# Optimization experiments

Measured on AMD Instinct MI355X. Metric: run time of the kernel, lower is better.

## Reference

```python
import jax, jax.numpy as jnp
import numpy as np

V_NUM = 4
NUM_HEADS = 8


def setup_inputs() -> dict:
    key = jax.random.key(0)
    k1, k2, k3 = jax.random.split(key, 3)
    B, C, H, W = 8, 512, 24, 24
    x = jax.random.normal(k1, (B, C, H, W), dtype=jnp.float32)
    # 1x1 conv weights stored as [out_ch, in_ch]
    w_qkv = jax.random.normal(k2, (3 * C, C), dtype=jnp.float32) * (C ** -0.5)
    w_proj = jax.random.normal(k3, (C, C), dtype=jnp.float32) * (C ** -0.5)
    b_proj = jnp.zeros((C,), dtype=jnp.float32)
    return {"x": x, "w_qkv": w_qkv, "w_proj": w_proj, "b_proj": b_proj}


def reference(x, w_qkv, w_proj, b_proj):
    B, C, H, W = x.shape
    hd = C // NUM_HEADS          # head dim
    scale = hd ** -0.5
    g = B // V_NUM               # batch groups
    N = V_NUM * H * W            # tokens per group

    # 1x1 conv qkv (no bias): [B, 3C, H, W]
    qkv = jnp.einsum('bchw,oc->bohw', x, w_qkv)
    # [g, v, 3C, H, W] -> [g, 3C, v, H, W] -> [g, heads, 3*hd, N]
    t = qkv.reshape(g, V_NUM, 3 * C, H, W).transpose(0, 2, 1, 3, 4)
    t = t.reshape(g, NUM_HEADS, 3 * hd, N)
    q, k, v = jnp.split(t, 3, axis=2)  # each [g, heads, hd, N]

    # attn = k^T @ q * scale : [g, heads, N, N]
    attn = jnp.einsum('ghdn,ghdm->ghnm', k, q) * scale
    attn = jax.nn.softmax(attn, axis=-2)  # softmax over the k axis (dim=-2)

    # out = v @ attn : [g, heads, hd, N]
    out = jnp.einsum('ghdn,ghnm->ghdm', v, attn)
    # [g, C, v, H, W] -> [g, v, C, H, W] -> [B, C, H, W]
    out = out.reshape(g, C, V_NUM, H, W).transpose(0, 2, 1, 3, 4).reshape(B, C, H, W)

    # 1x1 conv proj with bias
    out = jnp.einsum('bchw,oc->bohw', out, w_proj) + b_proj[None, :, None, None]
    return out
```

## Files before the change

### kernel.cpp

```cpp
#include <hip/hip_runtime.h>
#include <stdint.h>

typedef _Float16 f16;
typedef _Float16 half8 __attribute__((ext_vector_type(8)));
typedef _Float16 half4 __attribute__((ext_vector_type(4)));
typedef float floatx4 __attribute__((ext_vector_type(4)));

#define LOG2E 1.44269504088896340736f

__device__ __forceinline__ void async_cp16(const void* g, void* l) {
  __builtin_amdgcn_global_load_lds((const __attribute__((address_space(1))) void*)g,
                                   (__attribute__((address_space(3))) void*)l, 16, 0, 0);
}

__global__ __launch_bounds__(256) void k_prep(const float* __restrict__ x,
                                              f16* __restrict__ XT,
                                              const float* __restrict__ wqkv,
                                              const float* __restrict__ wproj,
                                              f16* __restrict__ WQ, f16* __restrict__ WP) {
  __shared__ f16 sT[64][72];
  const int bid = blockIdx.x;
  const int tid = threadIdx.x;
  if (bid < 576) {
    const int hw0 = (bid % 9) * 64, c0 = ((bid / 9) & 7) * 64, b = bid / 72;
    const int cc = tid >> 6, hwc = tid & 63;
    const float* xb = x + (size_t)b * 294912;
    for (int i = 0; i < 16; ++i) {
      int c = c0 + i * 4 + cc;
      sT[hwc][i * 4 + cc] = (f16)xb[c * 576 + hw0 + hwc];
    }
    __syncthreads();
    const int c_c = tid & 63, rr = tid >> 6;
    f16* xtb = XT + ((size_t)b * 576 + hw0) * 512 + c0;
    for (int j = 0; j < 16; ++j) {
      int r = j * 4 + rr;
      xtb[(size_t)r * 512 + c_c] = sT[r][c_c];
    }
  } else {
    const float SCALE_Q = 0.125f * LOG2E;
    const int total1 = 1536 * 512, total2 = 512 * 512;
    for (int idx = (bid - 576) * 256 + tid; idx < total1 + total2; idx += 128 * 256) {
      if (idx < total1) {
        int row = idx >> 9;
        float v = wqkv[idx];
        if ((row % 192) < 64) v *= SCALE_Q;
        WQ[idx] = (f16)v;
      } else {
        WP[idx - total1] = (f16)wproj[idx - total1];
      }
    }
  }
}

__global__ __launch_bounds__(256) void k_qkv_gemm(const f16* __restrict__ XT,
                                                  const f16* __restrict__ WQ,
                                                  f16* __restrict__ Qh, f16* __restrict__ Kh,
                                                  f16* __restrict__ Vh) {
  const int t0 = blockIdx.x * 128, n0 = blockIdx.y * 128;
  __shared__ alignas(16) f16 smem[2 * 128 * 64];
  f16* sA = smem;
  f16* sB = smem + 128 * 64;
  const int tid = threadIdx.x;
  const int wave = tid >> 6, lane = tid & 63, quad = lane >> 4, l16 = lane & 15;
  const int msub = (wave & 1) * 64, nsub = (wave >> 1) * 64;
  const floatx4 fzero = {0.f, 0.f, 0.f, 0.f};
  floatx4 acc[4][4];
  for (int i = 0; i < 4; ++i)
    for (int j = 0; j < 4; ++j) acc[i][j] = fzero;

  for (int k0 = 0; k0 < 512; k0 += 64) {
    __syncthreads();
    for (int p = 0; p < 4; ++p) {
      int e = p * 256 + tid;
      int row = e >> 3, colb = e & 7;
      async_cp16((const char*)XT + ((size_t)(t0 + row) * 512 + k0 + colb * 8) * 2,
                 (char*)sA + e * 16);
      async_cp16((const char*)WQ + ((size_t)(n0 + row) * 512 + k0 + colb * 8) * 2,
                 (char*)sB + e * 16);
    }
    __syncthreads();
    for (int f = 0; f < 2; ++f) {
      half8 a[4], bfr[4];
      for (int ms = 0; ms < 4; ++ms)
        a[ms] = *(const half8*)&sA[(msub + ms * 16 + l16) * 64 + f * 32 + quad * 8];
      for (int ns = 0; ns < 4; ++ns)
        bfr[ns] = *(const half8*)&sB[(nsub + ns * 16 + l16) * 64 + f * 32 + quad * 8];
      for (int ms = 0; ms < 4; ++ms)
        for (int ns = 0; ns < 4; ++ns)
          acc[ms][ns] =
              __builtin_amdgcn_mfma_f32_16x16x32_f16(a[ms], bfr[ns], acc[ms][ns], 0, 0, 0);
    }
  }
  for (int ms = 0; ms < 4; ++ms) {
    int tbase = t0 + msub + ms * 16 + quad * 4;
    for (int ns = 0; ns < 4; ++ns) {
      int row = n0 + nsub + ns * 16 + l16;
      int h = row / 192, rr2 = row % 192;
      int sel = rr2 >> 6, d = rr2 & 63;
      if (sel == 2) continue;
      for (int r = 0; r < 4; ++r) {
        int t = tbase + r;
        int b = t / 576, hw = t % 576;
        int g = b >> 2, v = b & 3;
        int n = v * 576 + hw;
        int gh = g * 8 + h;
        f16 hv = (f16)acc[ms][ns][r];
        size_t idx = ((size_t)gh * 2304 + n) * 64 + d;
        if (sel == 0)
          Qh[idx] = hv;
        else
          Kh[idx] = hv;
      }
    }
  }
  const int r0 = n0 % 192;
  if (r0 != 0) {
    const int vloc = (r0 == 128) ? 0 : 64;
    const int h = (n0 + vloc) / 192;
    f16* sVT = smem;
    __syncthreads();
    if ((wave >> 1) == (vloc >> 6)) {
      for (int ms = 0; ms < 4; ++ms) {
        int tok = msub + ms * 16 + quad * 4;
        for (int ns = 0; ns < 4; ++ns) {
          int d = ns * 16 + l16;
          half4 hv;
          for (int r = 0; r < 4; ++r) hv[r] = (f16)acc[ms][ns][r];
          *(half4*)&sVT[d * 136 + tok] = hv;
        }
      }
    }
    __syncthreads();
    for (int pss = 0; pss < 4; ++pss) {
      int d = pss * 16 + (tid >> 4), chunk = tid & 15;
      int t = t0 + chunk * 8;
      int b = t / 576, hw = t - b * 576;
      int gh = (b >> 2) * 8 + h, n = (b & 3) * 576 + hw;
      *(half8*)(Vh + (size_t)gh * 147456 + (size_t)d * 2304 + n) =
          *(const half8*)&sVT[d * 136 + chunk * 8];
    }
  }
}

__global__ __launch_bounds__(384) void k_attn(const f16* __restrict__ Qh,
                                              const f16* __restrict__ Kh,
                                              const f16* __restrict__ Vh,
                                              f16* __restrict__ AOT) {
  const int mt = blockIdx.x, gh = blockIdx.y;
  const int m0 = mt * 64;
  const int g = gh >> 3, h = gh & 7;
  const f16* Qg = Qh + (size_t)gh * 147456;
  const f16* Kg = Kh + (size_t)gh * 147456;
  const f16* Vg = Vh + (size_t)gh * 147456;
  __shared__ alignas(16) f16 smem[24576];
  f16* sK = smem;
  f16* sV = smem + 12288;
  const int tid = threadIdx.x;
  const int wave = tid >> 6, lane = tid & 63, quad = lane >> 4, l16 = lane & 15;
  const int wq = wave & 1, str = wave >> 1;
  const floatx4 fzero = {0.f, 0.f, 0.f, 0.f};
  const int sw = l16 & 7;
  const int vsw = (l16 >> 1) & 3;

  auto stage_kv = [&](int ktile, int buf) {
#pragma unroll
    for (int p = 0; p < 4; ++p) {
      int idx = p * 384 + tid;
      int isV = idx >= 768;
      int rem = isV ? idx - 768 : idx;
      int qt = rem >> 8, unit = rem & 255;
      if (!isV) {
        int row = unit >> 3, cb = unit & 7;
        async_cp16(Kg + (size_t)(qt * 768 + ktile * 32 + row) * 64 + ((cb ^ (row & 7)) << 3),
                   (char*)(sK + (qt * 2 + buf) * 2048) + unit * 16);
      } else {
        int row = unit >> 2, cb = unit & 3;
        async_cp16(
            Vg + (size_t)row * 2304 + qt * 768 + ktile * 32 + ((cb ^ ((row >> 1) & 3)) << 3),
            (char*)(sV + (qt * 2 + buf) * 2048) + unit * 16);
      }
    }
  };

  half8 qa[2][2];
#pragma unroll
  for (int s = 0; s < 2; ++s) {
    int qrow = m0 + wq * 32 + s * 16 + l16;
    qa[s][0] = *(const half8*)(Qg + (size_t)qrow * 64 + quad * 8);
    qa[s][1] = *(const half8*)(Qg + (size_t)qrow * 64 + 32 + quad * 8);
  }

  stage_kv(0, 0);
  __syncthreads();
  stage_kv(1, 1);

  float l_lane[2] = {0.f, 0.f};
  floatx4 o[2][4];
  for (int s = 0; s < 2; ++s)
    for (int dt = 0; dt < 4; ++dt) o[s][dt] = fzero;

  for (int kt = 0; kt < 24; ++kt) {
    const f16* bK = sK + (str * 2 + (kt & 1)) * 2048;
    const f16* bV = sV + (str * 2 + (kt & 1)) * 2048;

    half4 pf[2][2];
#pragma unroll
    for (int nt = 0; nt < 2; ++nt) {
      int krow = nt * 16 + l16;
      half8 kb0 = *(const half8*)&bK[krow * 64 + ((quad ^ sw) << 3)];
      half8 kb1 = *(const half8*)&bK[krow * 64 + (((4 + quad) ^ sw) << 3)];
#pragma unroll
      for (int s = 0; s < 2; ++s) {
        floatx4 t = __builtin_amdgcn_mfma_f32_16x16x32_f16(kb0, qa[s][0], fzero, 0, 0, 0);
        t = __builtin_amdgcn_mfma_f32_16x16x32_f16(kb1, qa[s][1], t, 0, 0, 0);
#pragma unroll
        for (int r = 0; r < 4; ++r) {
          float e = __builtin_amdgcn_exp2f(t[r]);
          l_lane[s] += e;
          pf[s][nt][r] = (f16)e;
        }
      }
    }
#pragma unroll
    for (int dt = 0; dt < 4; ++dt) {
      int vrow = dt * 16 + l16;
#pragma unroll
      for (int nt = 0; nt < 2; ++nt) {
        int chunk = nt * 2 + (quad >> 1);
        half4 vb = *(const half4*)&bV[vrow * 32 + ((chunk ^ vsw) << 3) + (quad & 1) * 4];
#pragma unroll
        for (int s = 0; s < 2; ++s)
          o[s][dt] = __builtin_amdgcn_mfma_f32_16x16x16f16(pf[s][nt], vb, o[s][dt], 0, 0, 0);
      }
    }

    if (kt < 23) {
      __syncthreads();
      if (kt + 2 < 24) stage_kv(kt + 2, kt & 1);
    }
  }

  __syncthreads();
  float* cO = (float*)smem;
  float* cL = (float*)(smem + 16384);
  if (str != 0) {
    int base = (str - 1) * 2 + wq;
#pragma unroll
    for (int s = 0; s < 2; ++s) {
      cL[(base * 2 + s) * 64 + lane] = l_lane[s];
      for (int dt = 0; dt < 4; ++dt)
        *(floatx4*)&cO[(((base * 2 + s) * 4 + dt) * 64 + lane) * 4] = o[s][dt];
    }
  }
  __syncthreads();
  if (str == 0) {
#pragma unroll
    for (int q2 = 0; q2 < 2; ++q2) {
      int base = q2 * 2 + wq;
      for (int s = 0; s < 2; ++s) {
        l_lane[s] += cL[(base * 2 + s) * 64 + lane];
        for (int dt = 0; dt < 4; ++dt)
          o[s][dt] += *(const floatx4*)&cO[(((base * 2 + s) * 4 + dt) * 64 + lane) * 4];
      }
    }
    for (int s = 0; s < 2; ++s) {
      l_lane[s] += __shfl_xor(l_lane[s], 16, 64);
      l_lane[s] += __shfl_xor(l_lane[s], 32, 64);
      float inv[4];
      for (int r = 0; r < 4; ++r) {
        float lr = __shfl(l_lane[s], quad * 4 + r, 64);
        inv[r] = 1.f / lr;
      }
      for (int dt = 0; dt < 4; ++dt)
        for (int r = 0; r < 4; ++r) {
          int n_tok = m0 + wq * 32 + s * 16 + quad * 4 + r;
          int v = n_tok / 576, hw = n_tok % 576;
          int bb = g * 4 + v;
          int c = h * 64 + dt * 16 + l16;
          AOT[((size_t)bb * 576 + hw) * 512 + c] = (f16)(o[s][dt][r] * inv[r]);
        }
    }
  }
}

__global__ __launch_bounds__(256) void k_proj_gemm(const f16* __restrict__ AOT,
                                                   const f16* __restrict__ WP,
                                                   const float* __restrict__ bias,
                                                   float* __restrict__ out) {
  const int o0 = blockIdx.x * 64, t0 = blockIdx.y * 128;
  __shared__ alignas(16) f16 sA[64 * 64];
  __shared__ alignas(16) f16 sB[128 * 64];
  const int tid = threadIdx.x;
  const int wave = tid >> 6, lane = tid & 63, quad = lane >> 4, l16 = lane & 15;
  const int msub = (wave & 1) * 32, nsub = (wave >> 1) * 64;
  const floatx4 fzero = {0.f, 0.f, 0.f, 0.f};
  floatx4 acc[2][4];
  for (int i = 0; i < 2; ++i)
    for (int j = 0; j < 4; ++j) acc[i][j] = fzero;

  for (int k0 = 0; k0 < 512; k0 += 64) {
    __syncthreads();
    for (int p = 0; p < 2; ++p) {
      int e = p * 256 + tid;
      int row = e >> 3, colb = e & 7;
      async_cp16((const char*)WP + ((size_t)(o0 + row) * 512 + k0 + colb * 8) * 2,
                 (char*)sA + e * 16);
    }
    for (int p = 0; p < 4; ++p) {
      int e = p * 256 + tid;
      int row = e >> 3, colb = e & 7;
      async_cp16((const char*)AOT + ((size_t)(t0 + row) * 512 + k0 + colb * 8) * 2,
                 (char*)sB + e * 16);
    }
    __syncthreads();
    for (int f = 0; f < 2; ++f) {
      half8 a[2], bfr[4];
      for (int ms = 0; ms < 2; ++ms)
        a[ms] = *(const half8*)&sA[(msub + ms * 16 + l16) * 64 + f * 32 + quad * 8];
      for (int ns = 0; ns < 4; ++ns)
        bfr[ns] = *(const half8*)&sB[(nsub + ns * 16 + l16) * 64 + f * 32 + quad * 8];
      for (int ms = 0; ms < 2; ++ms)
        for (int ns = 0; ns < 4; ++ns)
          acc[ms][ns] =
              __builtin_amdgcn_mfma_f32_16x16x32_f16(a[ms], bfr[ns], acc[ms][ns], 0, 0, 0);
    }
  }
  for (int ms = 0; ms < 2; ++ms) {
    int o_row = o0 + msub + ms * 16 + quad * 4;
    for (int ns = 0; ns < 4; ++ns) {
      int t = t0 + nsub + ns * 16 + l16;
      int b = t / 576, hw = t % 576;
      for (int r = 0; r < 4; ++r) {
        int orow = o_row + r;
        out[(size_t)b * 294912 + (size_t)orow * 576 + hw] = acc[ms][ns][r] + bias[orow];
      }
    }
  }
}

extern "C" void kernel_launch(void* const* d_in, const int* in_sizes, int n_in,
                              void* d_out, int out_size, void* d_ws, size_t ws_size,
                              hipStream_t stream) {
  const float* x = (const float*)d_in[0];
  const float* wqkv = (const float*)d_in[1];
  const float* wproj = (const float*)d_in[2];
  const float* bias = (const float*)d_in[3];
  float* out = (float*)d_out;
  char* ws = (char*)d_ws;
  f16* XT = (f16*)(ws + 0);
  f16* WQ = (f16*)(ws + 4718592);
  f16* WP = (f16*)(ws + 6291456);
  f16* Qh = (f16*)(ws + 6815744);
  f16* Kh = (f16*)(ws + 11534336);
  f16* Vh = (f16*)(ws + 16252928);
  f16* AOT = (f16*)(ws + 20971520);

  k_prep<<<dim3(704), dim3(256), 0, stream>>>(x, XT, wqkv, wproj, WQ, WP);
  k_qkv_gemm<<<dim3(36, 12), dim3(256), 0, stream>>>(XT, WQ, Qh, Kh, Vh);
  k_attn<<<dim3(36, 16), dim3(384), 0, stream>>>(Qh, Kh, Vh, AOT);
  k_proj_gemm<<<dim3(8, 36), dim3(256), 0, stream>>>(AOT, WP, bias, out);
}
```

Measured before the change: 156.7 us.

## Repartition attention block into 48-query tiles with two-way key split

Each attention block now handles 48 query rows split across three wave groups of 16 rows, with the key sequence split two ways instead of three, giving 768 blocks instead of 576. The goal is better CU occupancy and load balance on the device, plus a smaller LDS footprint per block. In exchange, each K/V tile loaded into LDS is reused by fewer query rows, so redundant K/V traffic rises. The longer serial loop over key tiles per wave also adds latency.

```diff
diff --git a/kernel.cpp b/kernel.cpp
--- a/kernel.cpp
+++ b/kernel.cpp
@@ -147,78 +147,76 @@
                                               const f16* __restrict__ Vh,
                                               f16* __restrict__ AOT) {
   const int mt = blockIdx.x, gh = blockIdx.y;
-  const int m0 = mt * 64;
+  const int m0 = mt * 48;
   const int g = gh >> 3, h = gh & 7;
   const f16* Qg = Qh + (size_t)gh * 147456;
   const f16* Kg = Kh + (size_t)gh * 147456;
   const f16* Vg = Vh + (size_t)gh * 147456;
-  __shared__ alignas(16) f16 smem[24576];
+  __shared__ alignas(16) f16 smem[16384];
   f16* sK = smem;
-  f16* sV = smem + 12288;
+  f16* sV = smem + 8192;
   const int tid = threadIdx.x;
   const int wave = tid >> 6, lane = tid & 63, quad = lane >> 4, l16 = lane & 15;
-  const int wq = wave & 1, str = wave >> 1;
+  const int str = wave & 1, qgrp = wave >> 1;
   const floatx4 fzero = {0.f, 0.f, 0.f, 0.f};
   const int sw = l16 & 7;
   const int vsw = (l16 >> 1) & 3;
 
   auto stage_kv = [&](int ktile, int buf) {
 #pragma unroll
-    for (int p = 0; p < 4; ++p) {
+    for (int p = 0; p < 3; ++p) {
       int idx = p * 384 + tid;
-      int isV = idx >= 768;
-      int rem = isV ? idx - 768 : idx;
-      int qt = rem >> 8, unit = rem & 255;
-      if (!isV) {
-        int row = unit >> 3, cb = unit & 7;
-        async_cp16(Kg + (size_t)(qt * 768 + ktile * 32 + row) * 64 + ((cb ^ (row & 7)) << 3),
-                   (char*)(sK + (qt * 2 + buf) * 2048) + unit * 16);
-      } else {
-        int row = unit >> 2, cb = unit & 3;
-        async_cp16(
-            Vg + (size_t)row * 2304 + qt * 768 + ktile * 32 + ((cb ^ ((row >> 1) & 3)) << 3),
-            (char*)(sV + (qt * 2 + buf) * 2048) + unit * 16);
+      if (idx < 1024) {
+        int isV = idx >= 512;
+        int rem = idx & 511;
+        int st = rem >> 8, unit = rem & 255;
+        if (!isV) {
+          int row = unit >> 3, cb = unit & 7;
+          async_cp16(
+              Kg + (size_t)(st * 1152 + ktile * 32 + row) * 64 + ((cb ^ (row & 7)) << 3),
+              (char*)(sK + (st * 2 + buf) * 2048) + unit * 16);
+        } else {
+          int row = unit >> 2, cb = unit & 3;
+          async_cp16(Vg + (size_t)row * 2304 + st * 1152 + ktile * 32 +
+                         ((cb ^ ((row >> 1) & 3)) << 3),
+                     (char*)(sV + (st * 2 + buf) * 2048) + unit * 16);
+        }
       }
     }
   };
 
-  half8 qa[2][2];
-#pragma unroll
-  for (int s = 0; s < 2; ++s) {
-    int qrow = m0 + wq * 32 + s * 16 + l16;
-    qa[s][0] = *(const half8*)(Qg + (size_t)qrow * 64 + quad * 8);
-    qa[s][1] = *(const half8*)(Qg + (size_t)qrow * 64 + 32 + quad * 8);
+  half8 qa[2];
+  {
+    int qrow = m0 + qgrp * 16 + l16;
+    qa[0] = *(const half8*)(Qg + (size_t)qrow * 64 + quad * 8);
+    qa[1] = *(const half8*)(Qg + (size_t)qrow * 64 + 32 + quad * 8);
   }
 
   stage_kv(0, 0);
   __syncthreads();
   stage_kv(1, 1);
 
-  float l_lane[2] = {0.f, 0.f};
-  floatx4 o[2][4];
-  for (int s = 0; s < 2; ++s)
-    for (int dt = 0; dt < 4; ++dt) o[s][dt] = fzero;
-
-  for (int kt = 0; kt < 24; ++kt) {
+  float l_lane = 0.f;
+  floatx4 o[4];
+  for (int dt = 0; dt < 4; ++dt) o[dt] = fzero;
+
+  for (int kt = 0; kt < 36; ++kt) {
     const f16* bK = sK + (str * 2 + (kt & 1)) * 2048;
     const f16* bV = sV + (str * 2 + (kt & 1)) * 2048;
 
-    half4 pf[2][2];
+    half4 pf[2];
 #pragma unroll
     for (int nt = 0; nt < 2; ++nt) {
       int krow = nt * 16 + l16;
       half8 kb0 = *(const half8*)&bK[krow * 64 + ((quad ^ sw) << 3)];
       half8 kb1 = *(const half8*)&bK[krow * 64 + (((4 + quad) ^ sw) << 3)];
-#pragma unroll
-      for (int s = 0; s < 2; ++s) {
-        floatx4 t = __builtin_amdgcn_mfma_f32_16x16x32_f16(kb0, qa[s][0], fzero, 0, 0, 0);
-        t = __builtin_amdgcn_mfma_f32_16x16x32_f16(kb1, qa[s][1], t, 0, 0, 0);
-#pragma unroll
-        for (int r = 0; r < 4; ++r) {
-          float e = __builtin_amdgcn_exp2f(t[r]);
-          l_lane[s] += e;
-          pf[s][nt][r] = (f16)e;
-        }
+      floatx4 t = __builtin_amdgcn_mfma_f32_16x16x32_f16(kb0, qa[0], fzero, 0, 0, 0);
+      t = __builtin_amdgcn_mfma_f32_16x16x32_f16(kb1, qa[1], t, 0, 0, 0);
+#pragma unroll
+      for (int r = 0; r < 4; ++r) {
+        float e = __builtin_amdgcn_exp2f(t[r]);
+        l_lane += e;
+        pf[nt][r] = (f16)e;
       }
     }
 #pragma unroll
@@ -228,58 +226,50 @@
       for (int nt = 0; nt < 2; ++nt) {
         int chunk = nt * 2 + (quad >> 1);
         half4 vb = *(const half4*)&bV[vrow * 32 + ((chunk ^ vsw) << 3) + (quad & 1) * 4];
-#pragma unroll
-        for (int s = 0; s < 2; ++s)
-          o[s][dt] = __builtin_amdgcn_mfma_f32_16x16x16f16(pf[s][nt], vb, o[s][dt], 0, 0, 0);
-      }
-    }
-
-    if (kt < 23) {
+        o[dt] = __builtin_amdgcn_mfma_f32_16x16x16f16(pf[nt], vb, o[dt], 0, 0, 0);
+      }
+    }
+
+    if (kt < 35) {
       __syncthreads();
-      if (kt + 2 < 24) stage_kv(kt + 2, kt & 1);
+      if (kt + 2 < 36) stage_kv(kt + 2, kt & 1);
     }
   }
 
   __syncthreads();
   float* cO = (float*)smem;
-  float* cL = (float*)(smem + 16384);
-  if (str != 0) {
-    int base = (str - 1) * 2 + wq;
-#pragma unroll
-    for (int s = 0; s < 2; ++s) {
-      cL[(base * 2 + s) * 64 + lane] = l_lane[s];
-      for (int dt = 0; dt < 4; ++dt)
-        *(floatx4*)&cO[(((base * 2 + s) * 4 + dt) * 64 + lane) * 4] = o[s][dt];
-    }
+  float* cL = (float*)(smem + 8192);
+  if (str == 1) {
+    cL[qgrp * 64 + lane] = l_lane;
+#pragma unroll
+    for (int dt = 0; dt < 4; ++dt)
+      *(floatx4*)&cO[((qgrp * 4 + dt) * 64 + lane) * 4] = o[dt];
   }
   __syncthreads();
   if (str == 0) {
-#pragma unroll
-    for (int q2 = 0; q2 < 2; ++q2) {
-      int base = q2 * 2 + wq;
-      for (int s = 0; s < 2; ++s) {
-        l_lane[s] += cL[(base * 2 + s) * 64 + lane];
-        for (int dt = 0; dt < 4; ++dt)
-          o[s][dt] += *(const floatx4*)&cO[(((base * 2 + s) * 4 + dt) * 64 + lane) * 4];
-      }
-    }
-    for (int s = 0; s < 2; ++s) {
-      l_lane[s] += __shfl_xor(l_lane[s], 16, 64);
-      l_lane[s] += __shfl_xor(l_lane[s], 32, 64);
-      float inv[4];
+    l_lane += cL[qgrp * 64 + lane];
+#pragma unroll
+    for (int dt = 0; dt < 4; ++dt)
+      o[dt] += *(const floatx4*)&cO[((qgrp * 4 + dt) * 64 + lane) * 4];
+
+    l_lane += __shfl_xor(l_lane, 16, 64);
+    l_lane += __shfl_xor(l_lane, 32, 64);
+    float inv[4];
+#pragma unroll
+    for (int r = 0; r < 4; ++r) {
+      float lr = __shfl(l_lane, quad * 4 + r, 64);
+      inv[r] = 1.f / lr;
+    }
+#pragma unroll
+    for (int dt = 0; dt < 4; ++dt)
+#pragma unroll
       for (int r = 0; r < 4; ++r) {
-        float lr = __shfl(l_lane[s], quad * 4 + r, 64);
-        inv[r] = 1.f / lr;
-      }
-      for (int dt = 0; dt < 4; ++dt)
-        for (int r = 0; r < 4; ++r) {
-          int n_tok = m0 + wq * 32 + s * 16 + quad * 4 + r;
-          int v = n_tok / 576, hw = n_tok % 576;
-          int bb = g * 4 + v;
-          int c = h * 64 + dt * 16 + l16;
-          AOT[((size_t)bb * 576 + hw) * 512 + c] = (f16)(o[s][dt][r] * inv[r]);
-        }
-    }
+        int n_tok = m0 + qgrp * 16 + quad * 4 + r;
+        int v = n_tok / 576, hw = n_tok % 576;
+        int bb = g * 4 + v;
+        int c = h * 64 + dt * 16 + l16;
+        AOT[((size_t)bb * 576 + hw) * 512 + c] = (f16)(o[dt][r] * inv[r]);
+      }
   }
 }
 
@@ -357,6 +347,6 @@
 
   k_prep<<<dim3(704), dim3(256), 0, stream>>>(x, XT, wqkv, wproj, WQ, WP);
   k_qkv_gemm<<<dim3(36, 12), dim3(256), 0, stream>>>(XT, WQ, Qh, Kh, Vh);
-  k_attn<<<dim3(36, 16), dim3(384), 0, stream>>>(Qh, Kh, Vh, AOT);
+  k_attn<<<dim3(48, 16), dim3(384), 0, stream>>>(Qh, Kh, Vh, AOT);
   k_proj_gemm<<<dim3(8, 36), dim3(256), 0, stream>>>(AOT, WP, bias, out);
 }
```

Measured after the change: 148.0 us. 1.06x faster.

## Retile attention into 48-query blocks with 2-way key split and uneven wave roles

Applied to the files above, without the earlier changes.

The attention kernel now processes 48 queries per block using 4 waves instead of 64 queries with 6 waves. The key dimension is split two ways instead of three, so each half runs 36 key tiles. Waves take unequal query shares (32 vs 16 rows), and the grid grows from 36x16 to 48x16 blocks with less shared memory per block. The aim is better occupancy and CU balance on 256 CUs, at the cost of a longer serial key loop per block and idle MFMA slots in the lighter waves.

```diff
diff --git a/kernel.cpp b/kernel.cpp
--- a/kernel.cpp
+++ b/kernel.cpp
@@ -142,22 +142,24 @@
   }
 }
 
-__global__ __launch_bounds__(384) void k_attn(const f16* __restrict__ Qh,
+__global__ __launch_bounds__(256) void k_attn(const f16* __restrict__ Qh,
                                               const f16* __restrict__ Kh,
                                               const f16* __restrict__ Vh,
                                               f16* __restrict__ AOT) {
   const int mt = blockIdx.x, gh = blockIdx.y;
-  const int m0 = mt * 64;
+  const int m0 = mt * 48;
   const int g = gh >> 3, h = gh & 7;
   const f16* Qg = Qh + (size_t)gh * 147456;
   const f16* Kg = Kh + (size_t)gh * 147456;
   const f16* Vg = Vh + (size_t)gh * 147456;
-  __shared__ alignas(16) f16 smem[24576];
+  __shared__ alignas(16) f16 smem[16384];
   f16* sK = smem;
-  f16* sV = smem + 12288;
+  f16* sV = smem + 8192;
   const int tid = threadIdx.x;
   const int wave = tid >> 6, lane = tid & 63, quad = lane >> 4, l16 = lane & 15;
-  const int wq = wave & 1, str = wave >> 1;
+  const int str = wave & 1, role = wave >> 1;
+  const int nsf = role ? 1 : 2;
+  const int qoff = role ? 32 : 0;
   const floatx4 fzero = {0.f, 0.f, 0.f, 0.f};
   const int sw = l16 & 7;
   const int vsw = (l16 >> 1) & 3;
@@ -165,19 +167,19 @@
   auto stage_kv = [&](int ktile, int buf) {
 #pragma unroll
     for (int p = 0; p < 4; ++p) {
-      int idx = p * 384 + tid;
-      int isV = idx >= 768;
-      int rem = isV ? idx - 768 : idx;
-      int qt = rem >> 8, unit = rem & 255;
+      int idx = p * 256 + tid;
+      int isV = idx >= 512;
+      int rem = idx & 511;
+      int st = rem >> 8, unit = rem & 255;
       if (!isV) {
         int row = unit >> 3, cb = unit & 7;
-        async_cp16(Kg + (size_t)(qt * 768 + ktile * 32 + row) * 64 + ((cb ^ (row & 7)) << 3),
-                   (char*)(sK + (qt * 2 + buf) * 2048) + unit * 16);
+        async_cp16(Kg + (size_t)(st * 1152 + ktile * 32 + row) * 64 + ((cb ^ (row & 7)) << 3),
+                   (char*)(sK + (st * 2 + buf) * 2048) + unit * 16);
       } else {
         int row = unit >> 2, cb = unit & 3;
-        async_cp16(
-            Vg + (size_t)row * 2304 + qt * 768 + ktile * 32 + ((cb ^ ((row >> 1) & 3)) << 3),
-            (char*)(sV + (qt * 2 + buf) * 2048) + unit * 16);
+        async_cp16(Vg + (size_t)row * 2304 + st * 1152 + ktile * 32 +
+                       ((cb ^ ((row >> 1) & 3)) << 3),
+                   (char*)(sV + (st * 2 + buf) * 2048) + unit * 16);
       }
     }
   };
@@ -185,9 +187,11 @@
   half8 qa[2][2];
 #pragma unroll
   for (int s = 0; s < 2; ++s) {
-    int qrow = m0 + wq * 32 + s * 16 + l16;
-    qa[s][0] = *(const half8*)(Qg + (size_t)qrow * 64 + quad * 8);
-    qa[s][1] = *(const half8*)(Qg + (size_t)qrow * 64 + 32 + quad * 8);
+    if (s < nsf) {
+      int qrow = m0 + qoff + s * 16 + l16;
+      qa[s][0] = *(const half8*)(Qg + (size_t)qrow * 64 + quad * 8);
+      qa[s][1] = *(const half8*)(Qg + (size_t)qrow * 64 + 32 + quad * 8);
+    }
   }
 
   stage_kv(0, 0);
@@ -199,7 +203,7 @@
   for (int s = 0; s < 2; ++s)
     for (int dt = 0; dt < 4; ++dt) o[s][dt] = fzero;
 
-  for (int kt = 0; kt < 24; ++kt) {
+  for (int kt = 0; kt < 36; ++kt) {
     const f16* bK = sK + (str * 2 + (kt & 1)) * 2048;
     const f16* bV = sV + (str * 2 + (kt & 1)) * 2048;
 
@@ -211,13 +215,15 @@
       half8 kb1 = *(const half8*)&bK[krow * 64 + (((4 + quad) ^ sw) << 3)];
 #pragma unroll
       for (int s = 0; s < 2; ++s) {
-        floatx4 t = __builtin_amdgcn_mfma_f32_16x16x32_f16(kb0, qa[s][0], fzero, 0, 0, 0);
-        t = __builtin_amdgcn_mfma_f32_16x16x32_f16(kb1, qa[s][1], t, 0, 0, 0);
-#pragma unroll
-        for (int r = 0; r < 4; ++r) {
-          float e = __builtin_amdgcn_exp2f(t[r]);
-          l_lane[s] += e;
-          pf[s][nt][r] = (f16)e;
+        if (s < nsf) {
+          floatx4 t = __builtin_amdgcn_mfma_f32_16x16x32_f16(kb0, qa[s][0], fzero, 0, 0, 0);
+          t = __builtin_amdgcn_mfma_f32_16x16x32_f16(kb1, qa[s][1], t, 0, 0, 0);
+#pragma unroll
+          for (int r = 0; r < 4; ++r) {
+            float e = __builtin_amdgcn_exp2f(t[r]);
+            l_lane[s] += e;
+            pf[s][nt][r] = (f16)e;
+          }
         }
       }
     }
@@ -230,55 +236,58 @@
         half4 vb = *(const half4*)&bV[vrow * 32 + ((chunk ^ vsw) << 3) + (quad & 1) * 4];
 #pragma unroll
         for (int s = 0; s < 2; ++s)
-          o[s][dt] = __builtin_amdgcn_mfma_f32_16x16x16f16(pf[s][nt], vb, o[s][dt], 0, 0, 0);
-      }
-    }
-
-    if (kt < 23) {
+          if (s < nsf)
+            o[s][dt] = __builtin_amdgcn_mfma_f32_16x16x16f16(pf[s][nt], vb, o[s][dt], 0, 0, 0);
+      }
+    }
+
+    if (kt < 35) {
       __syncthreads();
-      if (kt + 2 < 24) stage_kv(kt + 2, kt & 1);
+      if (kt + 2 < 36) stage_kv(kt + 2, kt & 1);
     }
   }
 
   __syncthreads();
   float* cO = (float*)smem;
-  float* cL = (float*)(smem + 16384);
-  if (str != 0) {
-    int base = (str - 1) * 2 + wq;
+  float* cL = (float*)(smem + 8192);
+  if (str == 1) {
 #pragma unroll
     for (int s = 0; s < 2; ++s) {
-      cL[(base * 2 + s) * 64 + lane] = l_lane[s];
-      for (int dt = 0; dt < 4; ++dt)
-        *(floatx4*)&cO[(((base * 2 + s) * 4 + dt) * 64 + lane) * 4] = o[s][dt];
+      if (s < nsf) {
+        int slot = role * 2 + s;
+        cL[slot * 64 + lane] = l_lane[s];
+        for (int dt = 0; dt < 4; ++dt)
+          *(floatx4*)&cO[((slot * 4 + dt) * 64 + lane) * 4] = o[s][dt];
+      }
     }
   }
   __syncthreads();
   if (str == 0) {
 #pragma unroll
-    for (int q2 = 0; q2 < 2; ++q2) {
-      int base = q2 * 2 + wq;
-      for (int s = 0; s < 2; ++s) {
-        l_lane[s] += cL[(base * 2 + s) * 64 + lane];
+    for (int s = 0; s < 2; ++s) {
+      if (s < nsf) {
+        int slot = role * 2 + s;
+        l_lane[s] += cL[slot * 64 + lane];
         for (int dt = 0; dt < 4; ++dt)
-          o[s][dt] += *(const floatx4*)&cO[(((base * 2 + s) * 4 + dt) * 64 + lane) * 4];
-      }
-    }
-    for (int s = 0; s < 2; ++s) {
-      l_lane[s] += __shfl_xor(l_lane[s], 16, 64);
-      l_lane[s] += __shfl_xor(l_lane[s], 32, 64);
-      float inv[4];
-      for (int r = 0; r < 4; ++r) {
-        float lr = __shfl(l_lane[s], quad * 4 + r, 64);
-        inv[r] = 1.f / lr;
-      }
-      for (int dt = 0; dt < 4; ++dt)
+          o[s][dt] += *(const floatx4*)&cO[((slot * 4 + dt) * 64 + lane) * 4];
+
+        float ls = l_lane[s];
+        ls += __shfl_xor(ls, 16, 64);
+        ls += __shfl_xor(ls, 32, 64);
+        float inv[4];
         for (int r = 0; r < 4; ++r) {
-          int n_tok = m0 + wq * 32 + s * 16 + quad * 4 + r;
-          int v = n_tok / 576, hw = n_tok % 576;
-          int bb = g * 4 + v;
-          int c = h * 64 + dt * 16 + l16;
-          AOT[((size_t)bb * 576 + hw) * 512 + c] = (f16)(o[s][dt][r] * inv[r]);
+          float lr = __shfl(ls, quad * 4 + r, 64);
+          inv[r] = 1.f / lr;
         }
+        for (int dt = 0; dt < 4; ++dt)
+          for (int r = 0; r < 4; ++r) {
+            int n_tok = m0 + qoff + s * 16 + quad * 4 + r;
+            int v = n_tok / 576, hw = n_tok % 576;
+            int bb = g * 4 + v;
+            int c = h * 64 + dt * 16 + l16;
+            AOT[((size_t)bb * 576 + hw) * 512 + c] = (f16)(o[s][dt][r] * inv[r]);
+          }
+      }
     }
   }
 }
@@ -357,6 +366,6 @@
 
   k_prep<<<dim3(704), dim3(256), 0, stream>>>(x, XT, wqkv, wproj, WQ, WP);
   k_qkv_gemm<<<dim3(36, 12), dim3(256), 0, stream>>>(XT, WQ, Qh, Kh, Vh);
-  k_attn<<<dim3(36, 16), dim3(384), 0, stream>>>(Qh, Kh, Vh, AOT);
+  k_attn<<<dim3(48, 16), dim3(256), 0, stream>>>(Qh, Kh, Vh, AOT);
   k_proj_gemm<<<dim3(8, 36), dim3(256), 0, stream>>>(AOT, WP, bias, out);
 }
```

Result: faster. 151.3 us (-3.5%).
